# Optimization experiments

Hardware: AMD Instinct MI355X
Metric: run time of the kernel (lower is better)

## Reference

```python
import jax, jax.numpy as jnp
import numpy as np
from jax import lax

S = 8192      # total tokens
HID = 1280    # hidden_size
H = 16        # num_heads
D = HID // H  # head_dim = 80
NSEG = 8      # number of equal-length segments (images)


def rotate_half(x):
    half = x.shape[-1] // 2
    return jnp.concatenate([-x[..., half:], x[..., :half]], axis=-1)


def setup_inputs() -> dict:
    key = jax.random.key(0)
    k1, k2, k3, k4 = jax.random.split(key, 4)
    hidden_states = jax.random.normal(k1, (S, HID), dtype=jnp.float32)
    # rotary embeddings: angles repeated over both halves, as in standard vision RoPE
    theta = jax.random.uniform(k2, (S, D // 2), dtype=jnp.float32) * (2.0 * np.pi)
    freqs = jnp.concatenate([theta, theta], axis=-1)  # [S, D]
    cos = jnp.cos(freqs)
    sin = jnp.sin(freqs)
    qkv_kernel = jax.random.normal(k3, (HID, 3, H, D), dtype=jnp.float32) * 0.02
    qkv_bias = jnp.zeros((3, H, D), dtype=jnp.float32)
    proj_kernel = jax.random.normal(k4, (H * D, HID), dtype=jnp.float32) * 0.02
    proj_bias = jnp.zeros((HID,), dtype=jnp.float32)
    cu_seqlens = jnp.arange(NSEG + 1, dtype=jnp.int32) * (S // NSEG)
    return {
        "hidden_states": hidden_states, "cos": cos, "sin": sin,
        "qkv_kernel": qkv_kernel, "qkv_bias": qkv_bias,
        "proj_kernel": proj_kernel, "proj_bias": proj_bias,
        "cu_seqlens": cu_seqlens,
    }


def reference(hidden_states, cos, sin, qkv_kernel, qkv_bias, proj_kernel, proj_bias, cu_seqlens):
    P = lax.Precision.HIGHEST
    seq, dtype = hidden_states.shape[0], hidden_states.dtype
    # fused QKV projection: [S, 3, H, D]
    qkv = jnp.einsum('sd,dtnh->stnh', hidden_states, qkv_kernel, precision=P) + qkv_bias
    q, k, v = qkv[:, 0], qkv[:, 1], qkv[:, 2]
    # rotary position embedding in fp32 (as in original)
    cf = cos[:, None, :].astype(jnp.float32)
    sf = sin[:, None, :].astype(jnp.float32)
    qf = q.astype(jnp.float32)
    kf = k.astype(jnp.float32)
    q = (qf * cf + rotate_half(qf) * sf).astype(dtype)
    k = (kf * cf + rotate_half(kf) * sf).astype(dtype)
    # block-diagonal attention over equal-length segments from cu_seqlens
    n_seg = cu_seqlens.shape[0] - 1
    L = seq // n_seg  # segment length (uniform segments)
    head_dim = q.shape[-1]
    scale = head_dim ** (-0.5)
    qs = q.reshape(n_seg, L, H, head_dim)
    ks = k.reshape(n_seg, L, H, head_dim)
    vs = v.reshape(n_seg, L, H, head_dim)
    logits = jnp.einsum('bqhd,bkhd->bhqk', qs, ks, precision=P) * scale
    attn = jax.nn.softmax(logits.astype(jnp.float32), axis=-1).astype(dtype)
    out = jnp.einsum('bhqk,bkhd->bqhd', attn, vs, precision=P).reshape(seq, H * head_dim)
    return jnp.einsum('se,ed->sd', out, proj_kernel, precision=P) + proj_bias
```

## Files before the change

kernel.cpp:

```cpp
#include <hip/hip_runtime.h>

#define S_LEN 8192
#define HID   1280
#define NHEAD 16
#define HD    80
#define NQKV  3840
#define VTS   8256

#define GLOBAL_AS __attribute__((address_space(1)))
#define LDS_AS    __attribute__((address_space(3)))

typedef __attribute__((ext_vector_type(8))) short bf16x8;
typedef __attribute__((ext_vector_type(4))) float f32x4;
typedef __attribute__((ext_vector_type(4))) unsigned short u16x4;
typedef __attribute__((ext_vector_type(8))) unsigned short u16x8;
typedef __attribute__((ext_vector_type(2))) unsigned int u32x2;

__device__ __forceinline__ unsigned short f2bf(float f) {
    union { float f; unsigned int u; } v; v.f = f;
    unsigned int r = v.u + 0x7FFFu + ((v.u >> 16) & 1u);
    return (unsigned short)(r >> 16);
}
__device__ __forceinline__ float bf2f(unsigned short h) {
    union { unsigned int u; float f; } v; v.u = ((unsigned int)h) << 16;
    return v.f;
}
__device__ __forceinline__ unsigned int cvt_pk_bf16(float a, float b) {
    unsigned int r;
    asm("v_cvt_pk_bf16_f32 %0, %1, %2" : "=v"(r) : "v"(a), "v"(b));
    return r;
}

#define NB_CVT (S_LEN * HID / 4 / 256)
#define NB_W1X (NQKV / 32)
#define NB_W1  (NB_W1X * (HID / 32))
#define NB_W2X (HID / 32)
#define NB_W2  (NB_W2X * (HID / 32))

__global__ __launch_bounds__(256) void k_prep(
    const float* __restrict__ hidden, unsigned short* __restrict__ hb,
    unsigned short* __restrict__ vbz,
    const float* __restrict__ qkv_w, unsigned short* __restrict__ wqkvt,
    const float* __restrict__ proj_w, unsigned short* __restrict__ wprojt)
{
    __shared__ float T[32][33];
    int b = blockIdx.x;
    if (b < NB_CVT) {
        if (b == 0 && threadIdx.x < 4)
            ((u16x8*)vbz)[threadIdx.x] = (u16x8)(unsigned short)0;
        int i = b * 256 + threadIdx.x;
        f32x4 v = *(const f32x4*)&hidden[(size_t)i * 4];
        u16x4 o;
        o[0] = f2bf(v[0]); o[1] = f2bf(v[1]); o[2] = f2bf(v[2]); o[3] = f2bf(v[3]);
        *(u16x4*)&hb[(size_t)i * 4] = o;
        return;
    }
    b -= NB_CVT;
    const float* W; unsigned short* Wt; int R, C, bx, by;
    if (b < NB_W1) { W = qkv_w;  Wt = wqkvt;  R = HID; C = NQKV; bx = b % NB_W1X; by = b / NB_W1X; }
    else { b -= NB_W1; W = proj_w; Wt = wprojt; R = HID; C = HID;  bx = b % NB_W2X; by = b / NB_W2X; }
    int r0 = by * 32, c0 = bx * 32;
    int tr = threadIdx.x >> 3, tc = (threadIdx.x & 7) * 4;
    f32x4 v = *(const f32x4*)&W[(size_t)(r0 + tr) * C + c0 + tc];
    T[tr][tc + 0] = v[0]; T[tr][tc + 1] = v[1];
    T[tr][tc + 2] = v[2]; T[tr][tc + 3] = v[3];
    __syncthreads();
    int c = threadIdx.x >> 3, r4 = (threadIdx.x & 7) * 4;
    u16x4 o;
    o[0] = f2bf(T[r4 + 0][c]); o[1] = f2bf(T[r4 + 1][c]);
    o[2] = f2bf(T[r4 + 2][c]); o[3] = f2bf(T[r4 + 3][c]);
    *(u16x4*)&Wt[(size_t)(c0 + c) * R + r0 + r4] = o;
}

__global__ __launch_bounds__(512, 2) void k_qkv256(
    const unsigned short* __restrict__ A,
    const unsigned short* __restrict__ Bt,
    const float* __restrict__ bias,
    unsigned short* __restrict__ q0, unsigned short* __restrict__ k0p,
    unsigned short* __restrict__ vt)
{
    __shared__ __align__(16) unsigned short As[2][2][16][64][8];
    __shared__ __align__(16) unsigned short Bs[2][2][16][64][8];
    const int tid = threadIdx.x;
    const int w = tid >> 6, l = tid & 63;
    const int qg = l & 15, g = l >> 4;
    const int wm = w >> 2, wn = w & 3;
    const int wm8 = wm * 8, wn4 = wn * 4;

    const int bid = blockIdx.x;
    const int xcd = bid & 7, t = bid >> 3;
    const int bm0 = (xcd * 4 + (t & 3)) * 256;
    const int bn0 = (t >> 2) * 256;

    const unsigned short* ga = A + (size_t)(bm0 + w * 16 + qg) * HID + g * 8;
    const unsigned short* gb = Bt + (size_t)(bn0 + w * 16 + qg) * HID + g * 8;

#define SG_A(d, ks, kcol) do {                                                  \
    __builtin_amdgcn_global_load_lds((const GLOBAL_AS unsigned int*)(ga + (kcol)), \
        (LDS_AS unsigned int*)&As[d][ks][w][0][0], 16, 0, 0);                   \
    __builtin_amdgcn_global_load_lds((const GLOBAL_AS unsigned int*)(ga + (size_t)128 * HID + (kcol)), \
        (LDS_AS unsigned int*)&As[d][ks][8 + w][0][0], 16, 0, 0); } while (0)
#define SG_B(d, ks, kcol) do {                                                  \
    __builtin_amdgcn_global_load_lds((const GLOBAL_AS unsigned int*)(gb + (kcol)), \
        (LDS_AS unsigned int*)&Bs[d][ks][w][0][0], 16, 0, 0);                   \
    __builtin_amdgcn_global_load_lds((const GLOBAL_AS unsigned int*)(gb + (size_t)128 * HID + (kcol)), \
        (LDS_AS unsigned int*)&Bs[d][ks][8 + w][0][0], 16, 0, 0); } while (0)

#define RD_A4(d, ks, fb) do {                                                   \
    af[0] = *(const bf16x8*)&As[d][ks][wm8 + (fb) + 0][l][0];                   \
    af[1] = *(const bf16x8*)&As[d][ks][wm8 + (fb) + 1][l][0];                   \
    af[2] = *(const bf16x8*)&As[d][ks][wm8 + (fb) + 2][l][0];                   \
    af[3] = *(const bf16x8*)&As[d][ks][wm8 + (fb) + 3][l][0]; } while (0)
#define RD_B4(d, ks) do {                                                       \
    bf[0] = *(const bf16x8*)&Bs[d][ks][wn4 + 0][l][0];                          \
    bf[1] = *(const bf16x8*)&Bs[d][ks][wn4 + 1][l][0];                          \
    bf[2] = *(const bf16x8*)&Bs[d][ks][wn4 + 2][l][0];                          \
    bf[3] = *(const bf16x8*)&Bs[d][ks][wn4 + 3][l][0]; } while (0)

#define MFMAQ(base) do {                                                        \
    _Pragma("unroll")                                                           \
    for (int m = 0; m < 4; ++m)                                                 \
        _Pragma("unroll")                                                       \
        for (int n = 0; n < 4; ++n)                                             \
            acc[(base) + m][n] = __builtin_amdgcn_mfma_f32_16x16x32_bf16(       \
                af[m], bf[n], acc[(base) + m][n], 0, 0, 0); } while (0)

#define BARW() do { __builtin_amdgcn_s_barrier();                               \
    __builtin_amdgcn_s_setprio(1); } while (0)
#define BARC() do { __builtin_amdgcn_s_setprio(0);                              \
    __builtin_amdgcn_s_barrier();                                               \
    __builtin_amdgcn_sched_barrier(0); } while (0)
#define BARC_VM4() do { __builtin_amdgcn_s_setprio(0);                          \
    asm volatile("s_waitcnt vmcnt(4)" ::: "memory");                            \
    __builtin_amdgcn_s_barrier();                                               \
    __builtin_amdgcn_sched_barrier(0); } while (0)
#define BARC_VM0() do { __builtin_amdgcn_s_setprio(0);                          \
    asm volatile("s_waitcnt vmcnt(0)" ::: "memory");                            \
    __builtin_amdgcn_s_barrier();                                               \
    __builtin_amdgcn_sched_barrier(0); } while (0)

    f32x4 acc[8][4];
#pragma unroll
    for (int m = 0; m < 8; ++m)
#pragma unroll
        for (int n = 0; n < 4; ++n) acc[m][n] = (f32x4){0.f, 0.f, 0.f, 0.f};

    SG_A(0, 0, 0);  SG_B(0, 0, 0);
    SG_A(0, 1, 32); SG_B(0, 1, 32);
    SG_A(1, 0, 64); SG_B(1, 0, 64);
    asm volatile("s_waitcnt vmcnt(4)" ::: "memory");
    __builtin_amdgcn_s_barrier();
    __builtin_amdgcn_sched_barrier(0);

    const int NIT = HID / 128;
    for (int j = 0; j < NIT; ++j) {
        const bool st = (j + 1 < NIT);
        const int c1 = j * 128 + 96;
        const int c2 = j * 128 + 128;
        const int c2b = j * 128 + 160;
        const int c3 = j * 128 + 192;
        bf16x8 af[4], bf[4];

        RD_A4(0, 0, 0); RD_B4(0, 0);
        SG_A(1, 1, c1);
        BARW(); MFMAQ(0); BARC();
        RD_A4(0, 0, 4);
        SG_B(1, 1, c1);
        BARW(); MFMAQ(4); BARC();
        RD_A4(0, 1, 0); RD_B4(0, 1);
        if (st) SG_A(0, 0, c2);
        BARW(); MFMAQ(0); BARC();
        RD_A4(0, 1, 4);
        if (st) SG_B(0, 0, c2);
        BARW(); MFMAQ(4);
        if (st) BARC_VM4(); else BARC_VM0();
        RD_A4(1, 0, 0); RD_B4(1, 0);
        if (st) SG_A(0, 1, c2b);
        BARW(); MFMAQ(0); BARC();
        RD_A4(1, 0, 4);
        if (st) SG_B(0, 1, c2b);
        BARW(); MFMAQ(4); BARC();
        RD_A4(1, 1, 0); RD_B4(1, 1);
        if (st) SG_A(1, 0, c3);
        BARW(); MFMAQ(0); BARC();
        RD_A4(1, 1, 4);
        if (st) SG_B(1, 0, c3);
        BARW(); MFMAQ(4);
        if (st) BARC_VM4(); else BARC_VM0();
    }
#undef SG_A
#undef SG_B
#undef RD_A4
#undef RD_B4
#undef MFMAQ
#undef BARW
#undef BARC
#undef BARC_VM4
#undef BARC_VM0

    const int t3 = bn0 / HID;
    if (t3 < 2) {
        unsigned short* dst = (t3 == 0) ? q0 : k0p;
        const int colbase = bn0 - t3 * HID + wn * 64 + qg;
        float bv[4];
#pragma unroll
        for (int n = 0; n < 4; ++n) bv[n] = bias[bn0 + wn * 64 + n * 16 + qg];
#pragma unroll
        for (int m = 0; m < 8; ++m)
#pragma unroll
            for (int r = 0; r < 4; ++r) {
                const int row = bm0 + wm * 128 + m * 16 + g * 4 + r;
                unsigned short* drow = dst + (size_t)row * HID + colbase;
#pragma unroll
                for (int n = 0; n < 4; ++n)
                    drow[n * 16] = f2bf(acc[m][n][r] + bv[n]);
            }
    } else {
        const int colbase = bn0 - 2 * HID + wn * 64;
#pragma unroll
        for (int n = 0; n < 4; ++n) {
            const int vcol = colbase + n * 16 + qg;
            const float bv = bias[bn0 + wn * 64 + n * 16 + qg];
            unsigned short* dcol = vt + (size_t)vcol * VTS + bm0 + wm * 128 + g * 4;
#pragma unroll
            for (int m = 0; m < 8; ++m) {
                u16x4 o;
#pragma unroll
                for (int r = 0; r < 4; ++r) o[r] = f2bf(acc[m][n][r] + bv);
                *(u16x4*)&dcol[m * 16] = o;
            }
        }
    }
}

__global__ __launch_bounds__(256) void k_rope(
    unsigned short* __restrict__ qb, unsigned short* __restrict__ kb,
    const float* __restrict__ cosb, const float* __restrict__ sinb)
{
    const float SCQ = 0.11180339887498949f * 1.44269504088896340f;
    int idx = blockIdx.x * 256 + threadIdx.x;
    if (idx >= S_LEN * NHEAD * 5) return;
    int s = idx / 80;
    int rem = idx - s * 80;
    int nh = rem / 5, h8 = (rem - nh * 5) * 8;
    size_t base = (size_t)s * HID + nh * HD + h8;
    const int cbase = s * HD + h8;
    float c0[8], c1[8], s0[8], s1[8];
    *(f32x4*)&c0[0] = *(const f32x4*)&cosb[cbase];
    *(f32x4*)&c0[4] = *(const f32x4*)&cosb[cbase + 4];
    *(f32x4*)&c1[0] = *(const f32x4*)&cosb[cbase + 40];
    *(f32x4*)&c1[4] = *(const f32x4*)&cosb[cbase + 44];
    *(f32x4*)&s0[0] = *(const f32x4*)&sinb[cbase];
    *(f32x4*)&s0[4] = *(const f32x4*)&sinb[cbase + 4];
    *(f32x4*)&s1[0] = *(const f32x4*)&sinb[cbase + 40];
    *(f32x4*)&s1[4] = *(const f32x4*)&sinb[cbase + 44];
    u16x8 qa = *(const u16x8*)&qb[base];
    u16x8 qb8 = *(const u16x8*)&qb[base + 40];
    u16x8 ka = *(const u16x8*)&kb[base];
    u16x8 kb8 = *(const u16x8*)&kb[base + 40];
    u16x8 o0, o1, p0, p1;
#pragma unroll
    for (int j = 0; j < 8; ++j) {
        float qaf = bf2f(qa[j]), qbf = bf2f(qb8[j]);
        o0[j] = f2bf((qaf * c0[j] - qbf * s0[j]) * SCQ);
        o1[j] = f2bf((qbf * c1[j] + qaf * s1[j]) * SCQ);
        float kaf = bf2f(ka[j]), kbf = bf2f(kb8[j]);
        p0[j] = f2bf(kaf * c0[j] - kbf * s0[j]);
        p1[j] = f2bf(kbf * c1[j] + kaf * s1[j]);
    }
    *(u16x8*)&qb[base] = o0;
    *(u16x8*)&qb[base + 40] = o1;
    *(u16x8*)&kb[base] = p0;
    *(u16x8*)&kb[base + 40] = p1;
}

__global__ __launch_bounds__(256) void k_attn(
    const unsigned short* __restrict__ qb, const unsigned short* __restrict__ kbuf,
    const unsigned short* __restrict__ vt, unsigned short* __restrict__ ao)
{
    __shared__ __align__(16) unsigned short Ks[2][64][104];
    __shared__ __align__(16) unsigned short Vs[2][80][64];
    __shared__ __align__(16) unsigned short Pls[4][2][16][68];

    const int tid = threadIdx.x;
    const int w = tid >> 6, l = tid & 63;
    const int qg = l & 15, g = l >> 4;
    const int wb = w << 6;
    const int vxor = (qg & 7) << 4;

    const int b = blockIdx.x;
    const int xcd = b & 7, j = b >> 3;
    const int p = xcd * 16 + (j >> 3);
    const int qt = j & 7;
    const int seg = p >> 4, head = p & 15;
    const int row0 = seg * 1024 + qt * 128 + w * 32;
    const size_t hoff = (size_t)head * HD;
    const int vhead = head * HD;
    const int kb0 = seg * 1024;

#define STAGE(bi, kr0_)                                                        \
    {                                                                          \
        const int kr0s = (kr0_);                                               \
        _Pragma("unroll")                                                      \
        for (int i = 0; i < 4; ++i) {                                          \
            const int u = i * 256 + tid;                                       \
            if (u < 832) {                                                     \
                const int r = u / 13, cu = (u - r * 13) * 8;                   \
                __builtin_amdgcn_global_load_lds(                              \
                    (const GLOBAL_AS unsigned int*)&kbuf[(size_t)(kr0s + r) * HID + hoff + cu], \
                    (LDS_AS unsigned int*)((LDS_AS unsigned short*)&Ks[bi][0][0] + (size_t)(i * 256 + wb) * 8), \
                    16, 0, 0);                                                 \
            }                                                                  \
        }                                                                      \
        _Pragma("unroll")                                                      \
        for (int i = 0; i < 3; ++i) {                                          \
            const int u = i * 256 + tid;                                       \
            if (u < 640) {                                                     \
                const int r = u >> 3;                                          \
                const int cs = ((u & 7) * 16) ^ ((r & 7) << 4);                \
                __builtin_amdgcn_global_load_lds(                              \
                    (const GLOBAL_AS unsigned int*)&vt[(size_t)(vhead + r) * VTS + kr0s + (cs >> 1)], \
                    (LDS_AS unsigned int*)((LDS_AS unsigned short*)&Vs[bi][0][0] + (size_t)(i * 256 + wb) * 8), \
                    16, 0, 0);                                                 \
            }                                                                  \
        }                                                                      \
    }

#define COMPUTE(bi)                                                            \
    {                                                                          \
        f32x4 st[2][4];                                                        \
        _Pragma("unroll")                                                      \
        for (int s = 0; s < 2; ++s)                                            \
            _Pragma("unroll")                                                  \
            for (int kn = 0; kn < 4; ++kn) st[s][kn] = (f32x4){0.f, 0.f, 0.f, 0.f}; \
        __builtin_amdgcn_s_setprio(1);                                         \
        _Pragma("unroll")                                                      \
        for (int ks = 0; ks < 3; ++ks)                                         \
            _Pragma("unroll")                                                  \
            for (int kn = 0; kn < 4; ++kn) {                                   \
                bf16x8 kf = *(const bf16x8*)&Ks[bi][kn * 16 + qg][ks * 32 + g * 8]; \
                st[0][kn] = __builtin_amdgcn_mfma_f32_16x16x32_bf16(kf, qf[0][ks], st[0][kn], 0, 0, 0); \
                st[1][kn] = __builtin_amdgcn_mfma_f32_16x16x32_bf16(kf, qf[1][ks], st[1][kn], 0, 0, 0); \
            }                                                                  \
        __builtin_amdgcn_s_setprio(0);                                         \
        _Pragma("unroll")                                                      \
        for (int s = 0; s < 2; ++s) {                                          \
            float psum = 0.f;                                                  \
            _Pragma("unroll")                                                  \
            for (int kn = 0; kn < 4; ++kn) {                                   \
                float p0 = exp2f(st[s][kn][0]);                                \
                float p1 = exp2f(st[s][kn][1]);                                \
                float p2 = exp2f(st[s][kn][2]);                                \
                float p3 = exp2f(st[s][kn][3]);                                \
                psum += (p0 + p1) + (p2 + p3);                                 \
                u32x2 pk;                                                      \
                pk[0] = cvt_pk_bf16(p0, p1);                                   \
                pk[1] = cvt_pk_bf16(p2, p3);                                   \
                *(u32x2*)&Pls[w][s][qg][kn * 16 + g * 4] = pk;                 \
            }                                                                  \
            psum += __shfl_xor(psum, 16, 64);                                  \
            psum += __shfl_xor(psum, 32, 64);                                  \
            lsum[s] += psum;                                                   \
        }                                                                      \
        __builtin_amdgcn_s_setprio(1);                                         \
        _Pragma("unroll")                                                      \
        for (int ks = 0; ks < 2; ++ks) {                                       \
            bf16x8 pf0 = *(const bf16x8*)&Pls[w][0][qg][ks * 32 + g * 8];      \
            bf16x8 pf1 = *(const bf16x8*)&Pls[w][1][qg][ks * 32 + g * 8];      \
            _Pragma("unroll")                                                  \
            for (int d = 0; d < 5; ++d) {                                      \
                bf16x8 vf = *(const bf16x8*)((const unsigned short*)&Vs[bi][0][0] + \
                    (d * 16 + qg) * 64 + (((ks * 64 + g * 16) ^ vxor) >> 1));  \
                acc[0][d] = __builtin_amdgcn_mfma_f32_16x16x32_bf16(vf, pf0, acc[0][d], 0, 0, 0); \
                acc[1][d] = __builtin_amdgcn_mfma_f32_16x16x32_bf16(vf, pf1, acc[1][d], 0, 0, 0); \
            }                                                                  \
        }                                                                      \
        __builtin_amdgcn_s_setprio(0);                                         \
    }

    bf16x8 qf[2][3];
#pragma unroll
    for (int s = 0; s < 2; ++s)
#pragma unroll
        for (int ks = 0; ks < 3; ++ks) {
            if (ks < 2 || g < 2)
                qf[s][ks] = *(const bf16x8*)&qb[(size_t)(row0 + s * 16 + qg) * HID + hoff + ks * 32 + g * 8];
            else
                qf[s][ks] = (bf16x8)(short)0;
        }

    float lsum[2] = {0.f, 0.f};
    f32x4 acc[2][5];
#pragma unroll
    for (int s = 0; s < 2; ++s)
#pragma unroll
        for (int d = 0; d < 5; ++d) acc[s][d] = (f32x4){0.f, 0.f, 0.f, 0.f};

    STAGE(0, kb0);
    __syncthreads();
    for (int ch = 0; ch < 16; ch += 2) {
        if (ch + 1 < 16) STAGE(1, kb0 + (ch + 1) * 64);
        COMPUTE(0);
        __syncthreads();
        if (ch + 2 < 16) STAGE(0, kb0 + (ch + 2) * 64);
        COMPUTE(1);
        __syncthreads();
    }

#pragma unroll
    for (int s = 0; s < 2; ++s) {
        const float inv = 1.0f / lsum[s];
        const int orow = row0 + s * 16 + qg;
#pragma unroll
        for (int d = 0; d < 5; ++d) {
            u16x4 o;
#pragma unroll
            for (int r = 0; r < 4; ++r) o[r] = f2bf(acc[s][d][r] * inv);
            *(u16x4*)&ao[(size_t)orow * HID + hoff + d * 16 + g * 4] = o;
        }
    }
#undef STAGE
#undef COMPUTE
}

__global__ __launch_bounds__(256) void k_proj(
    const unsigned short* __restrict__ A,
    const unsigned short* __restrict__ Bt,
    const float* __restrict__ bias, float* __restrict__ out)
{
    __shared__ __align__(16) unsigned short As[128][32];
    __shared__ __align__(16) unsigned short Bs[128][32];
    const int tid = threadIdx.x;
    const int w = tid >> 6, l = tid & 63;
    const int qg = l & 15, g = l >> 4;
    const int wr = w >> 1, wc = w & 1;
    const int bid = blockIdx.x;
    const int xcd = bid & 7, t = bid >> 3;
    const int bm0 = (xcd * 8 + (t & 7)) * 128;
    const int bn0 = (t >> 3) * 128;

    f32x4 acc[4][4];
#pragma unroll
    for (int m = 0; m < 4; ++m)
#pragma unroll
        for (int n = 0; n < 4; ++n) acc[m][n] = (f32x4){0.f, 0.f, 0.f, 0.f};

    const int lr = l >> 2, lc = (l & 3) * 8;
    const unsigned short* ga = A + (size_t)(bm0 + w * 16 + lr) * HID + lc;
    const unsigned short* gb = Bt + (size_t)(bn0 + w * 16 + lr) * HID + lc;
    LDS_AS unsigned int* la0 = (LDS_AS unsigned int*)&As[w * 16][0];
    LDS_AS unsigned int* la1 = (LDS_AS unsigned int*)&As[w * 16 + 64][0];
    LDS_AS unsigned int* lb0 = (LDS_AS unsigned int*)&Bs[w * 16][0];
    LDS_AS unsigned int* lb1 = (LDS_AS unsigned int*)&Bs[w * 16 + 64][0];

    for (int k0 = 0; k0 < HID; k0 += 32) {
        __syncthreads();
        __builtin_amdgcn_global_load_lds((const GLOBAL_AS unsigned int*)(ga + k0), la0, 16, 0, 0);
        __builtin_amdgcn_global_load_lds((const GLOBAL_AS unsigned int*)(ga + (size_t)64 * HID + k0), la1, 16, 0, 0);
        __builtin_amdgcn_global_load_lds((const GLOBAL_AS unsigned int*)(gb + k0), lb0, 16, 0, 0);
        __builtin_amdgcn_global_load_lds((const GLOBAL_AS unsigned int*)(gb + (size_t)64 * HID + k0), lb1, 16, 0, 0);
        __syncthreads();
        bf16x8 af[4], bff[4];
#pragma unroll
        for (int m = 0; m < 4; ++m) af[m] = *(const bf16x8*)&As[wr * 64 + m * 16 + qg][g * 8];
#pragma unroll
        for (int n = 0; n < 4; ++n) bff[n] = *(const bf16x8*)&Bs[wc * 64 + n * 16 + qg][g * 8];
#pragma unroll
        for (int m = 0; m < 4; ++m)
#pragma unroll
            for (int n = 0; n < 4; ++n)
                acc[m][n] = __builtin_amdgcn_mfma_f32_16x16x32_bf16(af[m], bff[n], acc[m][n], 0, 0, 0);
    }

#pragma unroll
    for (int n = 0; n < 4; ++n) {
        const int col = bn0 + wc * 64 + n * 16 + qg;
        const float bv = bias[col];
#pragma unroll
        for (int m = 0; m < 4; ++m)
#pragma unroll
            for (int r = 0; r < 4; ++r) {
                const int row = bm0 + wr * 64 + m * 16 + g * 4 + r;
                out[(size_t)row * HID + col] = acc[m][n][r] + bv;
            }
    }
}

extern "C" void kernel_launch(void* const* d_in, const int* in_sizes, int n_in,
                              void* d_out, int out_size, void* d_ws, size_t ws_size,
                              hipStream_t stream)
{
    (void)in_sizes; (void)n_in; (void)out_size; (void)ws_size;
    const float* hidden = (const float*)d_in[0];
    const float* cosb   = (const float*)d_in[1];
    const float* sinb   = (const float*)d_in[2];
    const float* qkv_w  = (const float*)d_in[3];
    const float* qkv_b  = (const float*)d_in[4];
    const float* proj_w = (const float*)d_in[5];
    const float* proj_b = (const float*)d_in[6];

    float* out = (float*)d_out;
    unsigned short* ws = (unsigned short*)d_ws;
    const size_t n = (size_t)S_LEN * HID;
    unsigned short* hb     = ws;
    unsigned short* wqkvt  = hb + n;
    unsigned short* wprojt = wqkvt + (size_t)NQKV * HID;
    unsigned short* qb     = wprojt + (size_t)HID * HID;
    unsigned short* kb     = qb + n;
    unsigned short* vb     = kb + n;
    unsigned short* vt     = vb + n;
    unsigned short* aob    = vt + (size_t)NHEAD * HD * VTS;

    k_prep<<<NB_CVT + NB_W1 + NB_W2, 256, 0, stream>>>(
        hidden, hb, vb, qkv_w, wqkvt, proj_w, wprojt);

    k_qkv256<<<480, 512, 0, stream>>>(hb, wqkvt, qkv_b, qb, kb, vt);

    k_rope<<<(S_LEN * NHEAD * 5 + 255) / 256, 256, 0, stream>>>(qb, kb, cosb, sinb);

    k_attn<<<1024, 256, 0, stream>>>(qb, kb, vt, aob);

    k_proj<<<640, 256, 0, stream>>>(aob, wprojt, proj_b, out);
}
```

Before: 251.1 us.

## Double-buffer A fragments and drop per-step barrier in QKV GEMM pipeline

Restructures the QKV GEMM main loop so each step reads the next A fragment set from LDS into a second register buffer while the current MFMA group runs. It also replaces the two barriers per step with one vmcnt-gated barrier and peels the last iteration to drain the loads. The aim is to hide LDS read latency and cut barrier stalls, at the cost of more registers and tighter vmcnt accounting, which could cause hazards if the counts are wrong.

```diff
diff --git a/kernel.cpp b/kernel.cpp
--- a/kernel.cpp
+++ b/kernel.cpp
@@ -106,37 +106,31 @@
     __builtin_amdgcn_global_load_lds((const GLOBAL_AS unsigned int*)(gb + (size_t)128 * HID + (kcol)), \
         (LDS_AS unsigned int*)&Bs[d][ks][8 + w][0][0], 16, 0, 0); } while (0)
 
-#define RD_A4(d, ks, fb) do {                                                   \
-    af[0] = *(const bf16x8*)&As[d][ks][wm8 + (fb) + 0][l][0];                   \
-    af[1] = *(const bf16x8*)&As[d][ks][wm8 + (fb) + 1][l][0];                   \
-    af[2] = *(const bf16x8*)&As[d][ks][wm8 + (fb) + 2][l][0];                   \
-    af[3] = *(const bf16x8*)&As[d][ks][wm8 + (fb) + 3][l][0]; } while (0)
+#define RD_A4TO(dst, d, ks, fb) do {                                            \
+    dst[0] = *(const bf16x8*)&As[d][ks][wm8 + (fb) + 0][l][0];                  \
+    dst[1] = *(const bf16x8*)&As[d][ks][wm8 + (fb) + 1][l][0];                  \
+    dst[2] = *(const bf16x8*)&As[d][ks][wm8 + (fb) + 2][l][0];                  \
+    dst[3] = *(const bf16x8*)&As[d][ks][wm8 + (fb) + 3][l][0]; } while (0)
 #define RD_B4(d, ks) do {                                                       \
     bf[0] = *(const bf16x8*)&Bs[d][ks][wn4 + 0][l][0];                          \
     bf[1] = *(const bf16x8*)&Bs[d][ks][wn4 + 1][l][0];                          \
     bf[2] = *(const bf16x8*)&Bs[d][ks][wn4 + 2][l][0];                          \
     bf[3] = *(const bf16x8*)&Bs[d][ks][wn4 + 3][l][0]; } while (0)
 
-#define MFMAQ(base) do {                                                        \
+#define MFMAQ(A_, base) do {                                                    \
     _Pragma("unroll")                                                           \
     for (int m = 0; m < 4; ++m)                                                 \
         _Pragma("unroll")                                                       \
         for (int n = 0; n < 4; ++n)                                             \
             acc[(base) + m][n] = __builtin_amdgcn_mfma_f32_16x16x32_bf16(       \
-                af[m], bf[n], acc[(base) + m][n], 0, 0, 0); } while (0)
-
-#define BARW() do { __builtin_amdgcn_s_barrier();                               \
-    __builtin_amdgcn_s_setprio(1); } while (0)
-#define BARC() do { __builtin_amdgcn_s_setprio(0);                              \
+                A_[m], bf[n], acc[(base) + m][n], 0, 0, 0); } while (0)
+
+#define PRIO1 __builtin_amdgcn_s_setprio(1)
+#define PRIO0 __builtin_amdgcn_s_setprio(0)
+#define VMB(n) do { asm volatile("s_waitcnt vmcnt(" #n ")" ::: "memory");       \
     __builtin_amdgcn_s_barrier();                                               \
     __builtin_amdgcn_sched_barrier(0); } while (0)
-#define BARC_VM4() do { __builtin_amdgcn_s_setprio(0);                          \
-    asm volatile("s_waitcnt vmcnt(4)" ::: "memory");                            \
-    __builtin_amdgcn_s_barrier();                                               \
-    __builtin_amdgcn_sched_barrier(0); } while (0)
-#define BARC_VM0() do { __builtin_amdgcn_s_setprio(0);                          \
-    asm volatile("s_waitcnt vmcnt(0)" ::: "memory");                            \
-    __builtin_amdgcn_s_barrier();                                               \
+#define BARO() do { __builtin_amdgcn_s_barrier();                               \
     __builtin_amdgcn_sched_barrier(0); } while (0)
 
     f32x4 acc[8][4];
@@ -148,55 +142,64 @@
     SG_A(0, 0, 0);  SG_B(0, 0, 0);
     SG_A(0, 1, 32); SG_B(0, 1, 32);
     SG_A(1, 0, 64); SG_B(1, 0, 64);
-    asm volatile("s_waitcnt vmcnt(4)" ::: "memory");
+    asm volatile("s_waitcnt vmcnt(6)" ::: "memory");
     __builtin_amdgcn_s_barrier();
     __builtin_amdgcn_sched_barrier(0);
 
+    bf16x8 afA[4], afB[4], bf[4];
+    RD_A4TO(afA, 0, 0, 0);
+
     const int NIT = HID / 128;
-    for (int j = 0; j < NIT; ++j) {
-        const bool st = (j + 1 < NIT);
+    for (int j = 0; j < NIT - 1; ++j) {
         const int c1 = j * 128 + 96;
         const int c2 = j * 128 + 128;
         const int c2b = j * 128 + 160;
         const int c3 = j * 128 + 192;
-        bf16x8 af[4], bf[4];
-
-        RD_A4(0, 0, 0); RD_B4(0, 0);
-        SG_A(1, 1, c1);
-        BARW(); MFMAQ(0); BARC();
-        RD_A4(0, 0, 4);
-        SG_B(1, 1, c1);
-        BARW(); MFMAQ(4); BARC();
-        RD_A4(0, 1, 0); RD_B4(0, 1);
-        if (st) SG_A(0, 0, c2);
-        BARW(); MFMAQ(0); BARC();
-        RD_A4(0, 1, 4);
-        if (st) SG_B(0, 0, c2);
-        BARW(); MFMAQ(4);
-        if (st) BARC_VM4(); else BARC_VM0();
-        RD_A4(1, 0, 0); RD_B4(1, 0);
-        if (st) SG_A(0, 1, c2b);
-        BARW(); MFMAQ(0); BARC();
-        RD_A4(1, 0, 4);
-        if (st) SG_B(0, 1, c2b);
-        BARW(); MFMAQ(4); BARC();
-        RD_A4(1, 1, 0); RD_B4(1, 1);
-        if (st) SG_A(1, 0, c3);
-        BARW(); MFMAQ(0); BARC();
-        RD_A4(1, 1, 4);
-        if (st) SG_B(1, 0, c3);
-        BARW(); MFMAQ(4);
-        if (st) BARC_VM4(); else BARC_VM0();
+
+        RD_B4(0, 0); RD_A4TO(afB, 0, 0, 4); SG_A(1, 1, c1);
+        PRIO1; MFMAQ(afA, 0); PRIO0; VMB(6);
+        RD_A4TO(afA, 0, 1, 0); SG_B(1, 1, c1);
+        PRIO1; MFMAQ(afB, 4); PRIO0; VMB(6);
+        RD_B4(0, 1); RD_A4TO(afB, 0, 1, 4); SG_A(0, 0, c2);
+        PRIO1; MFMAQ(afA, 0); PRIO0; VMB(6);
+        RD_A4TO(afA, 1, 0, 0); SG_B(0, 0, c2);
+        PRIO1; MFMAQ(afB, 4); PRIO0; VMB(6);
+        RD_B4(1, 0); RD_A4TO(afB, 1, 0, 4); SG_A(0, 1, c2b);
+        PRIO1; MFMAQ(afA, 0); PRIO0; VMB(6);
+        RD_A4TO(afA, 1, 1, 0); SG_B(0, 1, c2b);
+        PRIO1; MFMAQ(afB, 4); PRIO0; VMB(6);
+        RD_B4(1, 1); RD_A4TO(afB, 1, 1, 4); SG_A(1, 0, c3);
+        PRIO1; MFMAQ(afA, 0); PRIO0; VMB(6);
+        RD_A4TO(afA, 0, 0, 0); SG_B(1, 0, c3);
+        PRIO1; MFMAQ(afB, 4); PRIO0; VMB(6);
+    }
+    {
+        const int c1 = (NIT - 1) * 128 + 96;
+        RD_B4(0, 0); RD_A4TO(afB, 0, 0, 4); SG_A(1, 1, c1);
+        PRIO1; MFMAQ(afA, 0); PRIO0; VMB(6);
+        RD_A4TO(afA, 0, 1, 0); SG_B(1, 1, c1);
+        PRIO1; MFMAQ(afB, 4); PRIO0; VMB(6);
+        RD_B4(0, 1); RD_A4TO(afB, 0, 1, 4);
+        PRIO1; MFMAQ(afA, 0); PRIO0; VMB(4);
+        RD_A4TO(afA, 1, 0, 0);
+        PRIO1; MFMAQ(afB, 4); PRIO0; VMB(2);
+        RD_B4(1, 0); RD_A4TO(afB, 1, 0, 4);
+        PRIO1; MFMAQ(afA, 0); PRIO0; VMB(0);
+        RD_A4TO(afA, 1, 1, 0);
+        PRIO1; MFMAQ(afB, 4); PRIO0; BARO();
+        RD_B4(1, 1); RD_A4TO(afB, 1, 1, 4);
+        PRIO1; MFMAQ(afA, 0); PRIO0; BARO();
+        PRIO1; MFMAQ(afB, 4); PRIO0;
     }
 #undef SG_A
 #undef SG_B
-#undef RD_A4
+#undef RD_A4TO
 #undef RD_B4
 #undef MFMAQ
-#undef BARW
-#undef BARC
-#undef BARC_VM4
-#undef BARC_VM0
+#undef PRIO1
+#undef PRIO0
+#undef VMB
+#undef BARO
 
     const int t3 = bn0 / HID;
     if (t3 < 2) {
```

After: 251.9 us. No clear change (+0.3%).

## Replace pipelined 256x256 QKV GEMM with simple 128x128 templated GEMM

Applied to the files above, without the earlier changes.

Swaps the hand-pipelined 256x256-tile QKV GEMM (double-buffered LDS, setprio, fine-grained barriers) for a simpler 128x128-tile single-buffer kernel. The same template also serves the output projection, with a fragment-major LDS layout replacing the old row-major one. This trades less data reuse per tile and no load/compute overlap for more blocks and lower per-block resources, and it consolidates code.

```diff
diff --git a/kernel.cpp b/kernel.cpp
--- a/kernel.cpp
+++ b/kernel.cpp
@@ -72,164 +72,109 @@
     *(u16x4*)&Wt[(size_t)(c0 + c) * R + r0 + r4] = o;
 }
 
-__global__ __launch_bounds__(512, 2) void k_qkv256(
+template<int MODE>
+__global__ __launch_bounds__(256) void k_gemm128(
     const unsigned short* __restrict__ A,
     const unsigned short* __restrict__ Bt,
     const float* __restrict__ bias,
     unsigned short* __restrict__ q0, unsigned short* __restrict__ k0p,
-    unsigned short* __restrict__ vt)
+    unsigned short* __restrict__ vt, float* __restrict__ fo)
 {
-    __shared__ __align__(16) unsigned short As[2][2][16][64][8];
-    __shared__ __align__(16) unsigned short Bs[2][2][16][64][8];
+    __shared__ __align__(16) unsigned short As[8][64][8];
+    __shared__ __align__(16) unsigned short Bs[8][64][8];
     const int tid = threadIdx.x;
     const int w = tid >> 6, l = tid & 63;
     const int qg = l & 15, g = l >> 4;
-    const int wm = w >> 2, wn = w & 3;
-    const int wm8 = wm * 8, wn4 = wn * 4;
+    const int wr = w >> 1, wc = w & 1;
 
     const int bid = blockIdx.x;
     const int xcd = bid & 7, t = bid >> 3;
-    const int bm0 = (xcd * 4 + (t & 3)) * 256;
-    const int bn0 = (t >> 2) * 256;
-
-    const unsigned short* ga = A + (size_t)(bm0 + w * 16 + qg) * HID + g * 8;
-    const unsigned short* gb = Bt + (size_t)(bn0 + w * 16 + qg) * HID + g * 8;
-
-#define SG_A(d, ks, kcol) do {                                                  \
-    __builtin_amdgcn_global_load_lds((const GLOBAL_AS unsigned int*)(ga + (kcol)), \
-        (LDS_AS unsigned int*)&As[d][ks][w][0][0], 16, 0, 0);                   \
-    __builtin_amdgcn_global_load_lds((const GLOBAL_AS unsigned int*)(ga + (size_t)128 * HID + (kcol)), \
-        (LDS_AS unsigned int*)&As[d][ks][8 + w][0][0], 16, 0, 0); } while (0)
-#define SG_B(d, ks, kcol) do {                                                  \
-    __builtin_amdgcn_global_load_lds((const GLOBAL_AS unsigned int*)(gb + (kcol)), \
-        (LDS_AS unsigned int*)&Bs[d][ks][w][0][0], 16, 0, 0);                   \
-    __builtin_amdgcn_global_load_lds((const GLOBAL_AS unsigned int*)(gb + (size_t)128 * HID + (kcol)), \
-        (LDS_AS unsigned int*)&Bs[d][ks][8 + w][0][0], 16, 0, 0); } while (0)
-
-#define RD_A4(d, ks, fb) do {                                                   \
-    af[0] = *(const bf16x8*)&As[d][ks][wm8 + (fb) + 0][l][0];                   \
-    af[1] = *(const bf16x8*)&As[d][ks][wm8 + (fb) + 1][l][0];                   \
-    af[2] = *(const bf16x8*)&As[d][ks][wm8 + (fb) + 2][l][0];                   \
-    af[3] = *(const bf16x8*)&As[d][ks][wm8 + (fb) + 3][l][0]; } while (0)
-#define RD_B4(d, ks) do {                                                       \
-    bf[0] = *(const bf16x8*)&Bs[d][ks][wn4 + 0][l][0];                          \
-    bf[1] = *(const bf16x8*)&Bs[d][ks][wn4 + 1][l][0];                          \
-    bf[2] = *(const bf16x8*)&Bs[d][ks][wn4 + 2][l][0];                          \
-    bf[3] = *(const bf16x8*)&Bs[d][ks][wn4 + 3][l][0]; } while (0)
-
-#define MFMAQ(base) do {                                                        \
-    _Pragma("unroll")                                                           \
-    for (int m = 0; m < 4; ++m)                                                 \
-        _Pragma("unroll")                                                       \
-        for (int n = 0; n < 4; ++n)                                             \
-            acc[(base) + m][n] = __builtin_amdgcn_mfma_f32_16x16x32_bf16(       \
-                af[m], bf[n], acc[(base) + m][n], 0, 0, 0); } while (0)
-
-#define BARW() do { __builtin_amdgcn_s_barrier();                               \
-    __builtin_amdgcn_s_setprio(1); } while (0)
-#define BARC() do { __builtin_amdgcn_s_setprio(0);                              \
-    __builtin_amdgcn_s_barrier();                                               \
-    __builtin_amdgcn_sched_barrier(0); } while (0)
-#define BARC_VM4() do { __builtin_amdgcn_s_setprio(0);                          \
-    asm volatile("s_waitcnt vmcnt(4)" ::: "memory");                            \
-    __builtin_amdgcn_s_barrier();                                               \
-    __builtin_amdgcn_sched_barrier(0); } while (0)
-#define BARC_VM0() do { __builtin_amdgcn_s_setprio(0);                          \
-    asm volatile("s_waitcnt vmcnt(0)" ::: "memory");                            \
-    __builtin_amdgcn_s_barrier();                                               \
-    __builtin_amdgcn_sched_barrier(0); } while (0)
-
-    f32x4 acc[8][4];
-#pragma unroll
-    for (int m = 0; m < 8; ++m)
+    const int bm0 = (xcd * 8 + (t & 7)) * 128;
+    const int bn0 = (t >> 3) * 128;
+
+    const unsigned short* ga0 = A + (size_t)(bm0 + w * 16 + qg) * HID + g * 8;
+    const unsigned short* ga1 = A + (size_t)(bm0 + (4 + w) * 16 + qg) * HID + g * 8;
+    const unsigned short* gb0 = Bt + (size_t)(bn0 + w * 16 + qg) * HID + g * 8;
+    const unsigned short* gb1 = Bt + (size_t)(bn0 + (4 + w) * 16 + qg) * HID + g * 8;
+
+#define SG(p, d) __builtin_amdgcn_global_load_lds(                              \
+    (const GLOBAL_AS unsigned int*)(p), (LDS_AS unsigned int*)(d), 16, 0, 0)
+
+    f32x4 acc[4][4];
+#pragma unroll
+    for (int m = 0; m < 4; ++m)
 #pragma unroll
         for (int n = 0; n < 4; ++n) acc[m][n] = (f32x4){0.f, 0.f, 0.f, 0.f};
 
-    SG_A(0, 0, 0);  SG_B(0, 0, 0);
-    SG_A(0, 1, 32); SG_B(0, 1, 32);
-    SG_A(1, 0, 64); SG_B(1, 0, 64);
-    asm volatile("s_waitcnt vmcnt(4)" ::: "memory");
-    __builtin_amdgcn_s_barrier();
-    __builtin_amdgcn_sched_barrier(0);
-
-    const int NIT = HID / 128;
-    for (int j = 0; j < NIT; ++j) {
-        const bool st = (j + 1 < NIT);
-        const int c1 = j * 128 + 96;
-        const int c2 = j * 128 + 128;
-        const int c2b = j * 128 + 160;
-        const int c3 = j * 128 + 192;
-        bf16x8 af[4], bf[4];
-
-        RD_A4(0, 0, 0); RD_B4(0, 0);
-        SG_A(1, 1, c1);
-        BARW(); MFMAQ(0); BARC();
-        RD_A4(0, 0, 4);
-        SG_B(1, 1, c1);
-        BARW(); MFMAQ(4); BARC();
-        RD_A4(0, 1, 0); RD_B4(0, 1);
-        if (st) SG_A(0, 0, c2);
-        BARW(); MFMAQ(0); BARC();
-        RD_A4(0, 1, 4);
-        if (st) SG_B(0, 0, c2);
-        BARW(); MFMAQ(4);
-        if (st) BARC_VM4(); else BARC_VM0();
-        RD_A4(1, 0, 0); RD_B4(1, 0);
-        if (st) SG_A(0, 1, c2b);
-        BARW(); MFMAQ(0); BARC();
-        RD_A4(1, 0, 4);
-        if (st) SG_B(0, 1, c2b);
-        BARW(); MFMAQ(4); BARC();
-        RD_A4(1, 1, 0); RD_B4(1, 1);
-        if (st) SG_A(1, 0, c3);
-        BARW(); MFMAQ(0); BARC();
-        RD_A4(1, 1, 4);
-        if (st) SG_B(1, 0, c3);
-        BARW(); MFMAQ(4);
-        if (st) BARC_VM4(); else BARC_VM0();
-    }
-#undef SG_A
-#undef SG_B
-#undef RD_A4
-#undef RD_B4
-#undef MFMAQ
-#undef BARW
-#undef BARC
-#undef BARC_VM4
-#undef BARC_VM0
-
-    const int t3 = bn0 / HID;
-    if (t3 < 2) {
-        unsigned short* dst = (t3 == 0) ? q0 : k0p;
-        const int colbase = bn0 - t3 * HID + wn * 64 + qg;
-        float bv[4];
-#pragma unroll
-        for (int n = 0; n < 4; ++n) bv[n] = bias[bn0 + wn * 64 + n * 16 + qg];
-#pragma unroll
-        for (int m = 0; m < 8; ++m)
-#pragma unroll
-            for (int r = 0; r < 4; ++r) {
-                const int row = bm0 + wm * 128 + m * 16 + g * 4 + r;
-                unsigned short* drow = dst + (size_t)row * HID + colbase;
-#pragma unroll
-                for (int n = 0; n < 4; ++n)
-                    drow[n * 16] = f2bf(acc[m][n][r] + bv[n]);
-            }
-    } else {
-        const int colbase = bn0 - 2 * HID + wn * 64;
-#pragma unroll
-        for (int n = 0; n < 4; ++n) {
-            const int vcol = colbase + n * 16 + qg;
-            const float bv = bias[bn0 + wn * 64 + n * 16 + qg];
-            unsigned short* dcol = vt + (size_t)vcol * VTS + bm0 + wm * 128 + g * 4;
-#pragma unroll
-            for (int m = 0; m < 8; ++m) {
-                u16x4 o;
-#pragma unroll
-                for (int r = 0; r < 4; ++r) o[r] = f2bf(acc[m][n][r] + bv);
-                *(u16x4*)&dcol[m * 16] = o;
+    for (int k0 = 0; k0 < HID; k0 += 32) {
+        __syncthreads();
+        SG(ga0 + k0, &As[w][0][0]);
+        SG(ga1 + k0, &As[4 + w][0][0]);
+        SG(gb0 + k0, &Bs[w][0][0]);
+        SG(gb1 + k0, &Bs[4 + w][0][0]);
+        __syncthreads();
+        bf16x8 af[4], bff[4];
+#pragma unroll
+        for (int m = 0; m < 4; ++m) af[m] = *(const bf16x8*)&As[wr * 4 + m][l][0];
+#pragma unroll
+        for (int n = 0; n < 4; ++n) bff[n] = *(const bf16x8*)&Bs[wc * 4 + n][l][0];
+#pragma unroll
+        for (int m = 0; m < 4; ++m)
+#pragma unroll
+            for (int n = 0; n < 4; ++n)
+                acc[m][n] = __builtin_amdgcn_mfma_f32_16x16x32_bf16(af[m], bff[n], acc[m][n], 0, 0, 0);
+    }
+#undef SG
+
+    if constexpr (MODE == 0) {
+        const int t3 = bn0 / HID;
+        if (t3 < 2) {
+            unsigned short* dst = (t3 == 0) ? q0 : k0p;
+            const int colbase = bn0 - t3 * HID + wc * 64 + qg;
+            float bv[4];
+#pragma unroll
+            for (int n = 0; n < 4; ++n) bv[n] = bias[bn0 + wc * 64 + n * 16 + qg];
+#pragma unroll
+            for (int m = 0; m < 4; ++m)
+#pragma unroll
+                for (int r = 0; r < 4; ++r) {
+                    const int row = bm0 + wr * 64 + m * 16 + g * 4 + r;
+                    unsigned short* drow = dst + (size_t)row * HID + colbase;
+#pragma unroll
+                    for (int n = 0; n < 4; ++n)
+                        drow[n * 16] = f2bf(acc[m][n][r] + bv[n]);
+                }
+        } else {
+            const int colbase = bn0 - 2 * HID + wc * 64;
+#pragma unroll
+            for (int n = 0; n < 4; ++n) {
+                const int vcol = colbase + n * 16 + qg;
+                const float bv = bias[bn0 + wc * 64 + n * 16 + qg];
+                unsigned short* dcol = vt + (size_t)vcol * VTS + bm0 + wr * 64 + g * 4;
+#pragma unroll
+                for (int m = 0; m < 4; ++m) {
+                    u16x4 o;
+#pragma unroll
+                    for (int r = 0; r < 4; ++r) o[r] = f2bf(acc[m][n][r] + bv);
+                    *(u16x4*)&dcol[m * 16] = o;
+                }
             }
         }
+    } else {
+        const int colbase = bn0 + wc * 64 + qg;
+        float bv[4];
+#pragma unroll
+        for (int n = 0; n < 4; ++n) bv[n] = bias[bn0 + wc * 64 + n * 16 + qg];
+#pragma unroll
+        for (int m = 0; m < 4; ++m)
+#pragma unroll
+            for (int r = 0; r < 4; ++r) {
+                const int row = bm0 + wr * 64 + m * 16 + g * 4 + r;
+                float* orow = fo + (size_t)row * HID + colbase;
+#pragma unroll
+                for (int n = 0; n < 4; ++n)
+                    orow[n * 16] = acc[m][n][r] + bv[n];
+            }
     }
 }
 
@@ -423,69 +368,6 @@
 #undef COMPUTE
 }
 
-__global__ __launch_bounds__(256) void k_proj(
-    const unsigned short* __restrict__ A,
-    const unsigned short* __restrict__ Bt,
-    const float* __restrict__ bias, float* __restrict__ out)
-{
-    __shared__ __align__(16) unsigned short As[128][32];
-    __shared__ __align__(16) unsigned short Bs[128][32];
-    const int tid = threadIdx.x;
-    const int w = tid >> 6, l = tid & 63;
-    const int qg = l & 15, g = l >> 4;
-    const int wr = w >> 1, wc = w & 1;
-    const int bid = blockIdx.x;
-    const int xcd = bid & 7, t = bid >> 3;
-    const int bm0 = (xcd * 8 + (t & 7)) * 128;
-    const int bn0 = (t >> 3) * 128;
-
-    f32x4 acc[4][4];
-#pragma unroll
-    for (int m = 0; m < 4; ++m)
-#pragma unroll
-        for (int n = 0; n < 4; ++n) acc[m][n] = (f32x4){0.f, 0.f, 0.f, 0.f};
-
-    const int lr = l >> 2, lc = (l & 3) * 8;
-    const unsigned short* ga = A + (size_t)(bm0 + w * 16 + lr) * HID + lc;
-    const unsigned short* gb = Bt + (size_t)(bn0 + w * 16 + lr) * HID + lc;
-    LDS_AS unsigned int* la0 = (LDS_AS unsigned int*)&As[w * 16][0];
-    LDS_AS unsigned int* la1 = (LDS_AS unsigned int*)&As[w * 16 + 64][0];
-    LDS_AS unsigned int* lb0 = (LDS_AS unsigned int*)&Bs[w * 16][0];
-    LDS_AS unsigned int* lb1 = (LDS_AS unsigned int*)&Bs[w * 16 + 64][0];
-
-    for (int k0 = 0; k0 < HID; k0 += 32) {
-        __syncthreads();
-        __builtin_amdgcn_global_load_lds((const GLOBAL_AS unsigned int*)(ga + k0), la0, 16, 0, 0);
-        __builtin_amdgcn_global_load_lds((const GLOBAL_AS unsigned int*)(ga + (size_t)64 * HID + k0), la1, 16, 0, 0);
-        __builtin_amdgcn_global_load_lds((const GLOBAL_AS unsigned int*)(gb + k0), lb0, 16, 0, 0);
-        __builtin_amdgcn_global_load_lds((const GLOBAL_AS unsigned int*)(gb + (size_t)64 * HID + k0), lb1, 16, 0, 0);
-        __syncthreads();
-        bf16x8 af[4], bff[4];
-#pragma unroll
-        for (int m = 0; m < 4; ++m) af[m] = *(const bf16x8*)&As[wr * 64 + m * 16 + qg][g * 8];
-#pragma unroll
-        for (int n = 0; n < 4; ++n) bff[n] = *(const bf16x8*)&Bs[wc * 64 + n * 16 + qg][g * 8];
-#pragma unroll
-        for (int m = 0; m < 4; ++m)
-#pragma unroll
-            for (int n = 0; n < 4; ++n)
-                acc[m][n] = __builtin_amdgcn_mfma_f32_16x16x32_bf16(af[m], bff[n], acc[m][n], 0, 0, 0);
-    }
-
-#pragma unroll
-    for (int n = 0; n < 4; ++n) {
-        const int col = bn0 + wc * 64 + n * 16 + qg;
-        const float bv = bias[col];
-#pragma unroll
-        for (int m = 0; m < 4; ++m)
-#pragma unroll
-            for (int r = 0; r < 4; ++r) {
-                const int row = bm0 + wr * 64 + m * 16 + g * 4 + r;
-                out[(size_t)row * HID + col] = acc[m][n][r] + bv;
-            }
-    }
-}
-
 extern "C" void kernel_launch(void* const* d_in, const int* in_sizes, int n_in,
                               void* d_out, int out_size, void* d_ws, size_t ws_size,
                               hipStream_t stream)
@@ -514,11 +396,11 @@
     k_prep<<<NB_CVT + NB_W1 + NB_W2, 256, 0, stream>>>(
         hidden, hb, vb, qkv_w, wqkvt, proj_w, wprojt);
 
-    k_qkv256<<<480, 512, 0, stream>>>(hb, wqkvt, qkv_b, qb, kb, vt);
+    k_gemm128<0><<<1920, 256, 0, stream>>>(hb, wqkvt, qkv_b, qb, kb, vt, nullptr);
 
     k_rope<<<(S_LEN * NHEAD * 5 + 255) / 256, 256, 0, stream>>>(qb, kb, cosb, sinb);
 
     k_attn<<<1024, 256, 0, stream>>>(qb, kb, vt, aob);
 
-    k_proj<<<640, 256, 0, stream>>>(aob, wprojt, proj_b, out);
-}
+    k_gemm128<1><<<640, 256, 0, stream>>>(aob, wprojt, proj_b, nullptr, nullptr, nullptr, out);
+}
```

After: 335.6 us. +33.7%, slower.
